# Kernel optimization log

Measured on AMD Instinct MI355X. Metric: run time of the kernel, lower is better.

Reference implementation:

```python
import jax, jax.numpy as jnp
import numpy as np

D_MODEL = 1024
NUM_HEADS = 16
D_K = D_MODEL // NUM_HEADS


def setup_inputs() -> dict:
    key = jax.random.key(0)
    ks = jax.random.split(key, 5)
    s = 1.0 / np.sqrt(D_MODEL)
    return {
        "x": jax.random.normal(ks[0], (2, 2048, D_MODEL), dtype=jnp.float32),
        "Wq": jax.random.normal(ks[1], (D_MODEL, D_MODEL), dtype=jnp.float32) * s,
        "bq": jnp.zeros((D_MODEL,), dtype=jnp.float32),
        "Wk": jax.random.normal(ks[2], (D_MODEL, D_MODEL), dtype=jnp.float32) * s,
        "bk": jnp.zeros((D_MODEL,), dtype=jnp.float32),
        "Wv": jax.random.normal(ks[3], (D_MODEL, D_MODEL), dtype=jnp.float32) * s,
        "bv": jnp.zeros((D_MODEL,), dtype=jnp.float32),
        "Wo": jax.random.normal(ks[4], (D_MODEL, D_MODEL), dtype=jnp.float32) * s,
        "bo": jnp.zeros((D_MODEL,), dtype=jnp.float32),
    }


def reference(x, Wq, bq, Wk, bk, Wv, bv, Wo, bo):
    B, S, D = x.shape
    H, dk = NUM_HEADS, D_K
    Q = x @ Wq + bq  # [B, S, D]
    K = x @ Wk + bk
    V = x @ Wv + bv
    # Faithful to the torch code: plain .view(B, H, S, dk) (NO transpose),
    # i.e. heads are carved out of the flattened (S*D) dim, not the feature dim.
    Q = Q.reshape(B, H, S, dk)
    K = K.reshape(B, H, S, dk)
    V = V.reshape(B, H, S, dk)
    scores = jnp.einsum("bhqd,bhkd->bhqk", Q, K) / jnp.sqrt(jnp.float32(dk))
    attn = jax.nn.softmax(scores, axis=-1)  # [B, H, S, S]
    ctx = jnp.einsum("bhqk,bhkd->bhqd", attn, V)  # [B, H, S, dk]
    out = ctx.reshape(B, S, D) @ Wo + bo
    return out  # dropout is identity in eval mode
```

## Files before the change

kernel.cpp:

```cpp
#include <hip/hip_runtime.h>
#include <hip/hip_bf16.h>
#include <math.h>

#define D_MODEL 1024
#define SEQ     2048
#define BATCH   2
#define NHEAD   16
#define DKH     64
#define BH      (BATCH * NHEAD)

typedef unsigned short u16;
typedef unsigned int   u32;
typedef __bf16 bf16x8 __attribute__((ext_vector_type(8)));
typedef float  f32x4  __attribute__((ext_vector_type(4)));

#define MFMA16(a, b, c) __builtin_amdgcn_mfma_f32_16x16x32_bf16((a), (b), (c), 0, 0, 0)
#define AS1 __attribute__((address_space(1)))
#define AS3 __attribute__((address_space(3)))

#define QSCALE 0.18033688f

__device__ __forceinline__ u16 f2bf(float x) {
    u32 u = __float_as_uint(x);
    u += 0x7fffu + ((u >> 16) & 1u);
    return (u16)(u >> 16);
}
__device__ __forceinline__ float bf2f(u16 b) {
    return __uint_as_float(((u32)b) << 16);
}
__device__ __forceinline__ void gl16(const u16* g, void* lds) {
    __builtin_amdgcn_global_load_lds((const AS1 u32*)g, (AS3 u32*)lds, 16, 0, 0);
}

__global__ __launch_bounds__(256) void conv_all(
    const float* __restrict__ x, u16* __restrict__ Xh, int n4,
    const float* __restrict__ W0, const float* __restrict__ W1,
    const float* __restrict__ W2, const float* __restrict__ W3,
    u16* __restrict__ H0, u16* __restrict__ L0, u16* __restrict__ H1, u16* __restrict__ L1,
    u16* __restrict__ H2, u16* __restrict__ L2, u16* __restrict__ H3, u16* __restrict__ L3)
{
    const int t = threadIdx.x;
    if ((int)blockIdx.x < 4096) {
        int i = blockIdx.x * 256 + t;
        if (i >= n4) return;
        float4 v = reinterpret_cast<const float4*>(x)[i];
        uint2 H;
        H.x = f2bf(v.x) | ((u32)f2bf(v.y) << 16);
        H.y = f2bf(v.z) | ((u32)f2bf(v.w) << 16);
        reinterpret_cast<uint2*>(Xh)[i] = H;
        return;
    }
    int id = blockIdx.x - 4096;
    int bx = id & 15, by = (id >> 4) & 15, bz = id >> 8;
    const float* W; u16 *Ht, *Lt;
    if (bz == 0)      { W = W0; Ht = H0; Lt = L0; }
    else if (bz == 1) { W = W1; Ht = H1; Lt = L1; }
    else if (bz == 2) { W = W2; Ht = H2; Lt = L2; }
    else              { W = W3; Ht = H3; Lt = L3; }

    __shared__ float T[64][65];
    const int n0 = bx * 64, k0 = by * 64;
    #pragma unroll
    for (int i = 0; i < 4; ++i) {
        int f = t + i * 256;
        int kr = f >> 4, ns = (f & 15) * 4;
        float4 v = *reinterpret_cast<const float4*>(&W[(size_t)(k0 + kr) * D_MODEL + n0 + ns]);
        T[kr][ns + 0] = v.x; T[kr][ns + 1] = v.y; T[kr][ns + 2] = v.z; T[kr][ns + 3] = v.w;
    }
    __syncthreads();
    #pragma unroll
    for (int i = 0; i < 4; ++i) {
        int f = t + i * 256;
        int nr = f >> 4, ks = (f & 15) * 4;
        u16 hh[4], ll[4];
        #pragma unroll
        for (int j = 0; j < 4; ++j) {
            float xv = T[ks + j][nr];
            u16 hb = f2bf(xv);
            hh[j] = hb;
            ll[j] = f2bf(xv - bf2f(hb));
        }
        uint2 H, L;
        H.x = hh[0] | ((u32)hh[1] << 16); H.y = hh[2] | ((u32)hh[3] << 16);
        L.x = ll[0] | ((u32)ll[1] << 16); L.y = ll[2] | ((u32)ll[3] << 16);
        size_t o = (size_t)(n0 + nr) * D_MODEL + k0 + ks;
        *reinterpret_cast<uint2*>(&Ht[o]) = H;
        *reinterpret_cast<uint2*>(&Lt[o]) = L;
    }
}

__global__ __launch_bounds__(512, 2) void gemm_qkv(
    const u16* __restrict__ AhG,
    const u16* __restrict__ Bqh, const u16* __restrict__ Bql,
    const u16* __restrict__ Bkh, const u16* __restrict__ Bkl,
    const u16* __restrict__ Bvh, const u16* __restrict__ Bvl,
    const float* __restrict__ bq, const float* __restrict__ bk, const float* __restrict__ bv,
    u16* __restrict__ Qb, u16* __restrict__ Kb, u16* __restrict__ Vb)
{
    constexpr int K = D_MODEL, N = D_MODEL;
    __shared__ u16 LB[2][28672];

    const int tid  = threadIdx.x;
    const int wv   = tid >> 6;
    const int lane = tid & 63;
    const int quad = lane >> 4;
    const int l16  = lane & 15;
    const int wm   = wv >> 1, wn = wv & 1;
    const int brow = blockIdx.y * 128, bcol = blockIdx.x * 128;

    const u16* sp[7];
    int sldb[7];
    #pragma unroll
    for (int j = 0; j < 7; ++j) {
        int c = wv * 7 + j, a = c >> 3, cc = c & 7;
        int row = cc * 16 + (lane >> 2);
        int gseg = (lane & 3) ^ ((lane >> 3) & 3);
        const u16* p;
        if (a == 0)      p = AhG;
        else if (a == 1) p = Bqh;
        else if (a == 2) p = Bql;
        else if (a == 3) p = Bkh;
        else if (a == 4) p = Bkl;
        else if (a == 5) p = Bvh;
        else             p = Bvl;
        int rbase = (a == 0) ? brow : bcol;
        sp[j]   = p + (size_t)(rbase + row) * K + gseg * 8;
        sldb[j] = a * 8192 + cc * 1024;
    }

    int aro[2], bro[4];
    #pragma unroll
    for (int i = 0; i < 2; ++i) {
        int mr = wm * 32 + i * 16 + l16;
        aro[i] = mr * 64 + ((quad ^ ((mr >> 1) & 3)) * 16);
    }
    #pragma unroll
    for (int i = 0; i < 4; ++i) {
        int nr = wn * 64 + i * 16 + l16;
        bro[i] = nr * 64 + ((quad ^ ((nr >> 1) & 3)) * 16);
    }

    f32x4 acc[3][2][4] = {};

    #pragma unroll
    for (int j = 0; j < 7; ++j)
        gl16(sp[j], (char*)LB[0] + sldb[j]);

    for (int it = 0; it < K / 32; ++it) {
        const int cur = it & 1;
        __syncthreads();
        if (it + 1 < K / 32) {
            const int nxt = cur ^ 1;
            const int k1 = (it + 1) * 32;
            #pragma unroll
            for (int j = 0; j < 7; ++j)
                gl16(sp[j] + k1, (char*)LB[nxt] + sldb[j]);
        }

        bf16x8 ah[2];
        #pragma unroll
        for (int i = 0; i < 2; ++i)
            ah[i] = *reinterpret_cast<const bf16x8*>((const char*)LB[cur] + aro[i]);
        #pragma unroll
        for (int m = 0; m < 3; ++m) {
            const int bbh = (1 + 2 * m) * 8192, bbl = (2 + 2 * m) * 8192;
            bf16x8 bh[4], bl[4];
            #pragma unroll
            for (int i = 0; i < 4; ++i) {
                bh[i] = *reinterpret_cast<const bf16x8*>((const char*)LB[cur] + bbh + bro[i]);
                bl[i] = *reinterpret_cast<const bf16x8*>((const char*)LB[cur] + bbl + bro[i]);
            }
            #pragma unroll
            for (int mi = 0; mi < 2; ++mi)
                #pragma unroll
                for (int ni = 0; ni < 4; ++ni) {
                    f32x4 c = acc[m][mi][ni];
                    c = MFMA16(ah[mi], bh[ni], c);
                    c = MFMA16(ah[mi], bl[ni], c);
                    acc[m][mi][ni] = c;
                }
        }
    }

    #pragma unroll
    for (int m = 0; m < 3; ++m) {
        const float* bias = (m == 0) ? bq : (m == 1) ? bk : bv;
        u16* out = (m == 0) ? Qb : (m == 1) ? Kb : Vb;
        const float sc = (m == 0) ? QSCALE : 1.0f;
        #pragma unroll
        for (int mi = 0; mi < 2; ++mi) {
            #pragma unroll
            for (int ni = 0; ni < 4; ++ni) {
                int col = bcol + wn * 64 + ni * 16 + l16;
                float bvv = bias[col];
                #pragma unroll
                for (int r = 0; r < 4; ++r) {
                    int row = brow + wm * 32 + mi * 16 + quad * 4 + r;
                    out[(size_t)row * N + col] = f2bf((acc[m][mi][ni][r] + bvv) * sc);
                }
            }
        }
    }
}

__global__ __launch_bounds__(512, 2) void gemm_oproj(
    const u16* __restrict__ AhG, const u16* __restrict__ Bh, const u16* __restrict__ Bl,
    const float* __restrict__ bias, float* __restrict__ Cf)
{
    constexpr int K = D_MODEL, N = D_MODEL;
    __shared__ u16 LB[2][12288];

    const int tid  = threadIdx.x;
    const int wv   = tid >> 6;
    const int lane = tid & 63;
    const int quad = lane >> 4;
    const int l16  = lane & 15;
    const int wm   = wv >> 1, wn = wv & 1;
    const int brow = blockIdx.y * 128, bcol = blockIdx.x * 128;

    const u16* sp[3];
    int sldb[3];
    #pragma unroll
    for (int j = 0; j < 3; ++j) {
        int c = wv * 3 + j, a = c >> 3, cc = c & 7;
        int row = cc * 16 + (lane >> 2);
        int gseg = (lane & 3) ^ ((lane >> 3) & 3);
        const u16* p = (a == 0) ? AhG : (a == 1) ? Bh : Bl;
        int rbase = (a == 0) ? brow : bcol;
        sp[j]   = p + (size_t)(rbase + row) * K + gseg * 8;
        sldb[j] = a * 8192 + cc * 1024;
    }

    int aro[2], bro[4];
    #pragma unroll
    for (int i = 0; i < 2; ++i) {
        int mr = wm * 32 + i * 16 + l16;
        aro[i] = mr * 64 + ((quad ^ ((mr >> 1) & 3)) * 16);
    }
    #pragma unroll
    for (int i = 0; i < 4; ++i) {
        int nr = wn * 64 + i * 16 + l16;
        bro[i] = nr * 64 + ((quad ^ ((nr >> 1) & 3)) * 16);
    }

    f32x4 acc[2][4] = {};

    #pragma unroll
    for (int j = 0; j < 3; ++j)
        gl16(sp[j], (char*)LB[0] + sldb[j]);

    for (int it = 0; it < K / 32; ++it) {
        const int cur = it & 1;
        __syncthreads();
        if (it + 1 < K / 32) {
            const int nxt = cur ^ 1;
            const int k1 = (it + 1) * 32;
            #pragma unroll
            for (int j = 0; j < 3; ++j)
                gl16(sp[j] + k1, (char*)LB[nxt] + sldb[j]);
        }

        bf16x8 ah[2], bh[4], bl[4];
        #pragma unroll
        for (int i = 0; i < 2; ++i)
            ah[i] = *reinterpret_cast<const bf16x8*>((const char*)LB[cur] + aro[i]);
        #pragma unroll
        for (int i = 0; i < 4; ++i) {
            bh[i] = *reinterpret_cast<const bf16x8*>((const char*)LB[cur] + 8192 + bro[i]);
            bl[i] = *reinterpret_cast<const bf16x8*>((const char*)LB[cur] + 16384 + bro[i]);
        }
        #pragma unroll
        for (int mi = 0; mi < 2; ++mi)
            #pragma unroll
            for (int ni = 0; ni < 4; ++ni) {
                f32x4 c = acc[mi][ni];
                c = MFMA16(ah[mi], bh[ni], c);
                c = MFMA16(ah[mi], bl[ni], c);
                acc[mi][ni] = c;
            }
    }

    #pragma unroll
    for (int mi = 0; mi < 2; ++mi) {
        #pragma unroll
        for (int ni = 0; ni < 4; ++ni) {
            int col = bcol + wn * 64 + ni * 16 + l16;
            float bvv = bias[col];
            #pragma unroll
            for (int r = 0; r < 4; ++r) {
                int row = brow + wm * 32 + mi * 16 + quad * 4 + r;
                Cf[(size_t)row * N + col] = acc[mi][ni][r] + bvv;
            }
        }
    }
}

__global__ __launch_bounds__(256) void v_transpose(
    const u16* __restrict__ V, u16* __restrict__ Vt)
{
    __shared__ u16 T[64][72];
    const int bh = blockIdx.y, st = blockIdx.x;
    const u16* src = V + ((size_t)bh * SEQ + (size_t)st * 64) * 64;
    const int t = threadIdx.x;
    #pragma unroll
    for (int i = 0; i < 2; ++i) {
        int c  = t + i * 256;
        int s  = c >> 3;
        int d0 = (c & 7) * 8;
        uint4 v = reinterpret_cast<const uint4*>(src)[c];
        u16 e[8];
        e[0] = (u16)(v.x & 0xffff); e[1] = (u16)(v.x >> 16);
        e[2] = (u16)(v.y & 0xffff); e[3] = (u16)(v.y >> 16);
        e[4] = (u16)(v.z & 0xffff); e[5] = (u16)(v.z >> 16);
        e[6] = (u16)(v.w & 0xffff); e[7] = (u16)(v.w >> 16);
        #pragma unroll
        for (int j = 0; j < 8; ++j) T[d0 + j][s] = e[j];
    }
    __syncthreads();
    const int d = t >> 2, seg = t & 3;
    u16* dst = Vt + (size_t)bh * 64 * SEQ + (size_t)d * SEQ + st * 64 + seg * 16;
    uint4 a = *reinterpret_cast<const uint4*>(&T[d][seg * 16]);
    uint4 b = *reinterpret_cast<const uint4*>(&T[d][seg * 16 + 8]);
    reinterpret_cast<uint4*>(dst)[0] = a;
    reinterpret_cast<uint4*>(dst)[1] = b;
}

__global__ __launch_bounds__(256, 2) void attn_mfma(
    const u16* __restrict__ Qb_g, const u16* __restrict__ Kb_g,
    const u16* __restrict__ Vt_g, u16* __restrict__ Ch_g)
{
    __shared__ u16 KVS[2][8192];
    __shared__ u16 Pb [128 * 72];

    const int tid  = threadIdx.x;
    const int wv   = tid >> 6;
    const int lane = tid & 63;
    const int quad = lane >> 4;
    const int l16  = lane & 15;
    const int id   = blockIdx.x;
    const int bh   = id & 31;
    const int qt   = id >> 5;

    const size_t qbase = ((size_t)bh * SEQ + (size_t)qt * 128) * 64;
    const size_t kbh   = (size_t)bh * SEQ * 64;
    const size_t vtbh  = (size_t)bh * 64 * SEQ;

    bf16x8 qf[2][2];
    #pragma unroll
    for (int sub = 0; sub < 2; ++sub)
        #pragma unroll
        for (int ks = 0; ks < 2; ++ks) {
            size_t o = qbase + (size_t)(wv * 32 + sub * 16 + l16) * 64 + ks * 32 + quad * 8;
            qf[sub][ks] = *reinterpret_cast<const bf16x8*>(Qb_g + o);
        }

    const u16* sp[4];
    size_t sstep[4];
    int sldb[4];
    #pragma unroll
    for (int j = 0; j < 4; ++j) {
        int c   = wv * 4 + j;
        int arr = c >> 3, cc = c & 7;
        int row = cc * 8 + (lane >> 3);
        int sg  = (lane & 7) ^ (row & 7);
        if (arr == 0) { sp[j] = Kb_g + kbh + (size_t)row * 64 + sg * 8;   sstep[j] = 4096; }
        else          { sp[j] = Vt_g + vtbh + (size_t)row * SEQ + sg * 8; sstep[j] = 64; }
        sldb[j] = arr * 8192 + cc * 1024;
    }

    int fro[4][2];
    #pragma unroll
    for (int t = 0; t < 4; ++t)
        #pragma unroll
        for (int ks = 0; ks < 2; ++ks)
            fro[t][ks] = (t * 16 + l16) * 128 + (((ks * 4 + quad) ^ (l16 & 7)) * 16);

    bf16x8 onesv;
    #pragma unroll
    for (int i = 0; i < 8; ++i) onesv[i] = (__bf16)1.0f;

    f32x4 oacc[2][4] = {};
    f32x4 lsum[2] = {};

    #pragma unroll
    for (int j = 0; j < 4; ++j)
        gl16(sp[j], (char*)KVS[0] + sldb[j]);

    for (int kt = 0; kt < SEQ / 64; ++kt) {
        const int cur = kt & 1;
        __syncthreads();
        if (kt + 1 < SEQ / 64) {
            const int nxt = cur ^ 1;
            #pragma unroll
            for (int j = 0; j < 4; ++j)
                gl16(sp[j] + (size_t)(kt + 1) * sstep[j], (char*)KVS[nxt] + sldb[j]);
        }

        f32x4 sacc[2][4] = {};
        #pragma unroll
        for (int t4 = 0; t4 < 4; ++t4) {
            bf16x8 kh[2];
            kh[0] = *reinterpret_cast<const bf16x8*>((const char*)KVS[cur] + fro[t4][0]);
            kh[1] = *reinterpret_cast<const bf16x8*>((const char*)KVS[cur] + fro[t4][1]);
            #pragma unroll
            for (int sub = 0; sub < 2; ++sub) {
                f32x4 a = sacc[sub][t4];
                a = MFMA16(qf[sub][0], kh[0], a);
                a = MFMA16(qf[sub][1], kh[1], a);
                sacc[sub][t4] = a;
            }
        }

        #pragma unroll
        for (int sub = 0; sub < 2; ++sub) {
            int rowb = wv * 32 + sub * 16 + quad * 4;
            #pragma unroll
            for (int r = 0; r < 4; ++r) {
                u32 u0 = __float_as_uint(__builtin_amdgcn_exp2f(sacc[sub][0][r]));
                u32 u1 = __float_as_uint(__builtin_amdgcn_exp2f(sacc[sub][1][r]));
                u32 u2 = __float_as_uint(__builtin_amdgcn_exp2f(sacc[sub][2][r]));
                u32 u3 = __float_as_uint(__builtin_amdgcn_exp2f(sacc[sub][3][r]));
                int ro = (rowb + r) * 72 + l16;
                Pb[ro +  0] = (u16)(u0 >> 16);
                Pb[ro + 16] = (u16)(u1 >> 16);
                Pb[ro + 32] = (u16)(u2 >> 16);
                Pb[ro + 48] = (u16)(u3 >> 16);
            }
        }

        bf16x8 bvf[4][2];
        #pragma unroll
        for (int dt = 0; dt < 4; ++dt) {
            bvf[dt][0] = *reinterpret_cast<const bf16x8*>((const char*)KVS[cur] + 8192 + fro[dt][0]);
            bvf[dt][1] = *reinterpret_cast<const bf16x8*>((const char*)KVS[cur] + 8192 + fro[dt][1]);
        }
        #pragma unroll
        for (int sub = 0; sub < 2; ++sub) {
            bf16x8 ap[2];
            #pragma unroll
            for (int ks = 0; ks < 2; ++ks)
                ap[ks] = *reinterpret_cast<const bf16x8*>(
                    &Pb[(wv * 32 + sub * 16 + l16) * 72 + ks * 32 + quad * 8]);
            #pragma unroll
            for (int dt = 0; dt < 4; ++dt) {
                oacc[sub][dt] = MFMA16(ap[0], bvf[dt][0], oacc[sub][dt]);
                oacc[sub][dt] = MFMA16(ap[1], bvf[dt][1], oacc[sub][dt]);
            }
            lsum[sub] = MFMA16(ap[0], onesv, lsum[sub]);
            lsum[sub] = MFMA16(ap[1], onesv, lsum[sub]);
        }
    }

    u16* Oh = Ch_g + qbase;
    #pragma unroll
    for (int sub = 0; sub < 2; ++sub) {
        float inv[4];
        #pragma unroll
        for (int r = 0; r < 4; ++r) inv[r] = 1.0f / lsum[sub][r];
        #pragma unroll
        for (int dt = 0; dt < 4; ++dt)
            #pragma unroll
            for (int r = 0; r < 4; ++r) {
                int row = wv * 32 + sub * 16 + quad * 4 + r;
                Oh[(size_t)row * 64 + dt * 16 + l16] = f2bf(oacc[sub][dt][r] * inv[r]);
            }
    }
}

extern "C" void kernel_launch(void* const* d_in, const int* in_sizes, int n_in,
                              void* d_out, int out_size, void* d_ws, size_t ws_size,
                              hipStream_t stream)
{
    const float* x  = (const float*)d_in[0];
    const float* Wq = (const float*)d_in[1];
    const float* bq = (const float*)d_in[2];
    const float* Wk = (const float*)d_in[3];
    const float* bk = (const float*)d_in[4];
    const float* Wv = (const float*)d_in[5];
    const float* bv = (const float*)d_in[6];
    const float* Wo = (const float*)d_in[7];
    const float* bo = (const float*)d_in[8];
    float* out = (float*)d_out;

    const int M = BATCH * SEQ;
    const int N = D_MODEL;
    const size_t NE = (size_t)M * N;
    const size_t NW = (size_t)N * N;

    u16* w16 = (u16*)d_ws;
    u16* Xh   = w16;
    u16* Qb   = Xh   + NE;
    u16* Kb   = Qb   + NE;
    u16* Vb   = Kb   + NE;
    u16* Vtb  = Vb   + NE;
    u16* Ctxh = Vtb  + NE;
    u16* WTqh = Ctxh + NE;
    u16* WTql = WTqh + NW;
    u16* WTkh = WTql + NW;
    u16* WTkl = WTkh + NW;
    u16* WTvh = WTkl + NW;
    u16* WTvl = WTvh + NW;
    u16* WToh = WTvl + NW;
    u16* WTol = WToh + NW;

    conv_all<<<dim3(4096 + 1024), dim3(256), 0, stream>>>(
        x, Xh, (int)(NE / 4),
        Wq, Wk, Wv, Wo, WTqh, WTql, WTkh, WTkl, WTvh, WTvl, WToh, WTol);

    gemm_qkv<<<dim3(N / 128, M / 128), dim3(512), 0, stream>>>(
        Xh, WTqh, WTql, WTkh, WTkl, WTvh, WTvl, bq, bk, bv, Qb, Kb, Vb);

    v_transpose<<<dim3(SEQ / 64, BH), dim3(256), 0, stream>>>(Vb, Vtb);

    attn_mfma<<<dim3((SEQ / 128) * BH), dim3(256), 0, stream>>>(Qb, Kb, Vtb, Ctxh);

    gemm_oproj<<<dim3(N / 128, M / 128), dim3(512), 0, stream>>>(
        Ctxh, WToh, WTol, bo, out);
}
```

Baseline: 223.5 us.

## Drop low-order weight split in QKV GEMM and load K/V directly in attention

The QKV projection now uses only the high bf16 part of each weight instead of a hi+lo split. This halves the MFMAs, the LDS footprint and the weight loads, and conversion no longer writes lo parts for Wq/Wk/Wv. The attention kernel removes its double-buffered LDS staging of K and V^T and reads MFMA fragments directly from global memory, so it no longer needs the K/V barriers. The risks are lower projection accuracy and repeated global/cache reads of K/V by each wave.

```diff
diff --git a/kernel.cpp b/kernel.cpp
--- a/kernel.cpp
+++ b/kernel.cpp
@@ -36,8 +36,8 @@
     const float* __restrict__ x, u16* __restrict__ Xh, int n4,
     const float* __restrict__ W0, const float* __restrict__ W1,
     const float* __restrict__ W2, const float* __restrict__ W3,
-    u16* __restrict__ H0, u16* __restrict__ L0, u16* __restrict__ H1, u16* __restrict__ L1,
-    u16* __restrict__ H2, u16* __restrict__ L2, u16* __restrict__ H3, u16* __restrict__ L3)
+    u16* __restrict__ Hq, u16* __restrict__ Hk, u16* __restrict__ Hv,
+    u16* __restrict__ Ho, u16* __restrict__ Lo)
 {
     const int t = threadIdx.x;
     if ((int)blockIdx.x < 4096) {
@@ -52,11 +52,11 @@
     }
     int id = blockIdx.x - 4096;
     int bx = id & 15, by = (id >> 4) & 15, bz = id >> 8;
-    const float* W; u16 *Ht, *Lt;
-    if (bz == 0)      { W = W0; Ht = H0; Lt = L0; }
-    else if (bz == 1) { W = W1; Ht = H1; Lt = L1; }
-    else if (bz == 2) { W = W2; Ht = H2; Lt = L2; }
-    else              { W = W3; Ht = H3; Lt = L3; }
+    const float* W; u16* Ht;
+    if (bz == 0)      { W = W0; Ht = Hq; }
+    else if (bz == 1) { W = W1; Ht = Hk; }
+    else if (bz == 2) { W = W2; Ht = Hv; }
+    else              { W = W3; Ht = Ho; }
 
     __shared__ float T[64][65];
     const int n0 = bx * 64, k0 = by * 64;
@@ -85,20 +85,18 @@
         L.x = ll[0] | ((u32)ll[1] << 16); L.y = ll[2] | ((u32)ll[3] << 16);
         size_t o = (size_t)(n0 + nr) * D_MODEL + k0 + ks;
         *reinterpret_cast<uint2*>(&Ht[o]) = H;
-        *reinterpret_cast<uint2*>(&Lt[o]) = L;
+        if (bz == 3) *reinterpret_cast<uint2*>(&Lo[o]) = L;
     }
 }
 
 __global__ __launch_bounds__(512, 2) void gemm_qkv(
     const u16* __restrict__ AhG,
-    const u16* __restrict__ Bqh, const u16* __restrict__ Bql,
-    const u16* __restrict__ Bkh, const u16* __restrict__ Bkl,
-    const u16* __restrict__ Bvh, const u16* __restrict__ Bvl,
+    const u16* __restrict__ Bqh, const u16* __restrict__ Bkh, const u16* __restrict__ Bvh,
     const float* __restrict__ bq, const float* __restrict__ bk, const float* __restrict__ bv,
     u16* __restrict__ Qb, u16* __restrict__ Kb, u16* __restrict__ Vb)
 {
     constexpr int K = D_MODEL, N = D_MODEL;
-    __shared__ u16 LB[2][28672];
+    __shared__ u16 LB[2][16384];
 
     const int tid  = threadIdx.x;
     const int wv   = tid >> 6;
@@ -108,21 +106,18 @@
     const int wm   = wv >> 1, wn = wv & 1;
     const int brow = blockIdx.y * 128, bcol = blockIdx.x * 128;
 
-    const u16* sp[7];
-    int sldb[7];
-    #pragma unroll
-    for (int j = 0; j < 7; ++j) {
-        int c = wv * 7 + j, a = c >> 3, cc = c & 7;
+    const u16* sp[4];
+    int sldb[4];
+    #pragma unroll
+    for (int j = 0; j < 4; ++j) {
+        int c = wv * 4 + j, a = c >> 3, cc = c & 7;
         int row = cc * 16 + (lane >> 2);
         int gseg = (lane & 3) ^ ((lane >> 3) & 3);
         const u16* p;
         if (a == 0)      p = AhG;
         else if (a == 1) p = Bqh;
-        else if (a == 2) p = Bql;
-        else if (a == 3) p = Bkh;
-        else if (a == 4) p = Bkl;
-        else if (a == 5) p = Bvh;
-        else             p = Bvl;
+        else if (a == 2) p = Bkh;
+        else             p = Bvh;
         int rbase = (a == 0) ? brow : bcol;
         sp[j]   = p + (size_t)(rbase + row) * K + gseg * 8;
         sldb[j] = a * 8192 + cc * 1024;
@@ -143,7 +138,7 @@
     f32x4 acc[3][2][4] = {};
 
     #pragma unroll
-    for (int j = 0; j < 7; ++j)
+    for (int j = 0; j < 4; ++j)
         gl16(sp[j], (char*)LB[0] + sldb[j]);
 
     for (int it = 0; it < K / 32; ++it) {
@@ -153,7 +148,7 @@
             const int nxt = cur ^ 1;
             const int k1 = (it + 1) * 32;
             #pragma unroll
-            for (int j = 0; j < 7; ++j)
+            for (int j = 0; j < 4; ++j)
                 gl16(sp[j] + k1, (char*)LB[nxt] + sldb[j]);
         }
 
@@ -163,22 +158,16 @@
             ah[i] = *reinterpret_cast<const bf16x8*>((const char*)LB[cur] + aro[i]);
         #pragma unroll
         for (int m = 0; m < 3; ++m) {
-            const int bbh = (1 + 2 * m) * 8192, bbl = (2 + 2 * m) * 8192;
-            bf16x8 bh[4], bl[4];
-            #pragma unroll
-            for (int i = 0; i < 4; ++i) {
-                bh[i] = *reinterpret_cast<const bf16x8*>((const char*)LB[cur] + bbh + bro[i]);
-                bl[i] = *reinterpret_cast<const bf16x8*>((const char*)LB[cur] + bbl + bro[i]);
-            }
+            const int bb = (1 + m) * 8192;
+            bf16x8 bh[4];
+            #pragma unroll
+            for (int i = 0; i < 4; ++i)
+                bh[i] = *reinterpret_cast<const bf16x8*>((const char*)LB[cur] + bb + bro[i]);
             #pragma unroll
             for (int mi = 0; mi < 2; ++mi)
                 #pragma unroll
-                for (int ni = 0; ni < 4; ++ni) {
-                    f32x4 c = acc[m][mi][ni];
-                    c = MFMA16(ah[mi], bh[ni], c);
-                    c = MFMA16(ah[mi], bl[ni], c);
-                    acc[m][mi][ni] = c;
-                }
+                for (int ni = 0; ni < 4; ++ni)
+                    acc[m][mi][ni] = MFMA16(ah[mi], bh[ni], acc[m][mi][ni]);
         }
     }
 
@@ -329,8 +318,7 @@
     const u16* __restrict__ Qb_g, const u16* __restrict__ Kb_g,
     const u16* __restrict__ Vt_g, u16* __restrict__ Ch_g)
 {
-    __shared__ u16 KVS[2][8192];
-    __shared__ u16 Pb [128 * 72];
+    __shared__ u16 Pb[128 * 72];
 
     const int tid  = threadIdx.x;
     const int wv   = tid >> 6;
@@ -342,8 +330,8 @@
     const int qt   = id >> 5;
 
     const size_t qbase = ((size_t)bh * SEQ + (size_t)qt * 128) * 64;
-    const size_t kbh   = (size_t)bh * SEQ * 64;
-    const size_t vtbh  = (size_t)bh * 64 * SEQ;
+    const u16* Kt = Kb_g + (size_t)bh * SEQ * 64;
+    const u16* Vh = Vt_g + (size_t)bh * 64 * SEQ;
 
     bf16x8 qf[2][2];
     #pragma unroll
@@ -354,26 +342,14 @@
             qf[sub][ks] = *reinterpret_cast<const bf16x8*>(Qb_g + o);
         }
 
-    const u16* sp[4];
-    size_t sstep[4];
-    int sldb[4];
-    #pragma unroll
-    for (int j = 0; j < 4; ++j) {
-        int c   = wv * 4 + j;
-        int arr = c >> 3, cc = c & 7;
-        int row = cc * 8 + (lane >> 3);
-        int sg  = (lane & 7) ^ (row & 7);
-        if (arr == 0) { sp[j] = Kb_g + kbh + (size_t)row * 64 + sg * 8;   sstep[j] = 4096; }
-        else          { sp[j] = Vt_g + vtbh + (size_t)row * SEQ + sg * 8; sstep[j] = 64; }
-        sldb[j] = arr * 8192 + cc * 1024;
-    }
-
-    int fro[4][2];
+    int kfo[4][2], vfo[4][2];
     #pragma unroll
     for (int t = 0; t < 4; ++t)
         #pragma unroll
-        for (int ks = 0; ks < 2; ++ks)
-            fro[t][ks] = (t * 16 + l16) * 128 + (((ks * 4 + quad) ^ (l16 & 7)) * 16);
+        for (int ks = 0; ks < 2; ++ks) {
+            kfo[t][ks] = (t * 16 + l16) * 64 + ks * 32 + quad * 8;
+            vfo[t][ks] = (t * 16 + l16) * SEQ + ks * 32 + quad * 8;
+        }
 
     bf16x8 onesv;
     #pragma unroll
@@ -382,31 +358,20 @@
     f32x4 oacc[2][4] = {};
     f32x4 lsum[2] = {};
 
-    #pragma unroll
-    for (int j = 0; j < 4; ++j)
-        gl16(sp[j], (char*)KVS[0] + sldb[j]);
-
     for (int kt = 0; kt < SEQ / 64; ++kt) {
-        const int cur = kt & 1;
-        __syncthreads();
-        if (kt + 1 < SEQ / 64) {
-            const int nxt = cur ^ 1;
-            #pragma unroll
-            for (int j = 0; j < 4; ++j)
-                gl16(sp[j] + (size_t)(kt + 1) * sstep[j], (char*)KVS[nxt] + sldb[j]);
-        }
+        const int kofs = kt * 64 * 64;
+        const int vofs = kt * 64;
 
         f32x4 sacc[2][4] = {};
         #pragma unroll
         for (int t4 = 0; t4 < 4; ++t4) {
-            bf16x8 kh[2];
-            kh[0] = *reinterpret_cast<const bf16x8*>((const char*)KVS[cur] + fro[t4][0]);
-            kh[1] = *reinterpret_cast<const bf16x8*>((const char*)KVS[cur] + fro[t4][1]);
+            bf16x8 kh0 = *reinterpret_cast<const bf16x8*>(Kt + kofs + kfo[t4][0]);
+            bf16x8 kh1 = *reinterpret_cast<const bf16x8*>(Kt + kofs + kfo[t4][1]);
             #pragma unroll
             for (int sub = 0; sub < 2; ++sub) {
                 f32x4 a = sacc[sub][t4];
-                a = MFMA16(qf[sub][0], kh[0], a);
-                a = MFMA16(qf[sub][1], kh[1], a);
+                a = MFMA16(qf[sub][0], kh0, a);
+                a = MFMA16(qf[sub][1], kh1, a);
                 sacc[sub][t4] = a;
             }
         }
@@ -428,26 +393,25 @@
             }
         }
 
-        bf16x8 bvf[4][2];
+        bf16x8 bv0[4], bv1[4];
         #pragma unroll
         for (int dt = 0; dt < 4; ++dt) {
-            bvf[dt][0] = *reinterpret_cast<const bf16x8*>((const char*)KVS[cur] + 8192 + fro[dt][0]);
-            bvf[dt][1] = *reinterpret_cast<const bf16x8*>((const char*)KVS[cur] + 8192 + fro[dt][1]);
+            bv0[dt] = *reinterpret_cast<const bf16x8*>(Vh + vofs + vfo[dt][0]);
+            bv1[dt] = *reinterpret_cast<const bf16x8*>(Vh + vofs + vfo[dt][1]);
         }
         #pragma unroll
         for (int sub = 0; sub < 2; ++sub) {
-            bf16x8 ap[2];
-            #pragma unroll
-            for (int ks = 0; ks < 2; ++ks)
-                ap[ks] = *reinterpret_cast<const bf16x8*>(
-                    &Pb[(wv * 32 + sub * 16 + l16) * 72 + ks * 32 + quad * 8]);
+            bf16x8 ap0 = *reinterpret_cast<const bf16x8*>(
+                &Pb[(wv * 32 + sub * 16 + l16) * 72 + 0 + quad * 8]);
+            bf16x8 ap1 = *reinterpret_cast<const bf16x8*>(
+                &Pb[(wv * 32 + sub * 16 + l16) * 72 + 32 + quad * 8]);
             #pragma unroll
             for (int dt = 0; dt < 4; ++dt) {
-                oacc[sub][dt] = MFMA16(ap[0], bvf[dt][0], oacc[sub][dt]);
-                oacc[sub][dt] = MFMA16(ap[1], bvf[dt][1], oacc[sub][dt]);
-            }
-            lsum[sub] = MFMA16(ap[0], onesv, lsum[sub]);
-            lsum[sub] = MFMA16(ap[1], onesv, lsum[sub]);
+                oacc[sub][dt] = MFMA16(ap0, bv0[dt], oacc[sub][dt]);
+                oacc[sub][dt] = MFMA16(ap1, bv1[dt], oacc[sub][dt]);
+            }
+            lsum[sub] = MFMA16(ap0, onesv, lsum[sub]);
+            lsum[sub] = MFMA16(ap1, onesv, lsum[sub]);
         }
     }
 
@@ -495,20 +459,17 @@
     u16* Vtb  = Vb   + NE;
     u16* Ctxh = Vtb  + NE;
     u16* WTqh = Ctxh + NE;
-    u16* WTql = WTqh + NW;
-    u16* WTkh = WTql + NW;
-    u16* WTkl = WTkh + NW;
-    u16* WTvh = WTkl + NW;
-    u16* WTvl = WTvh + NW;
-    u16* WToh = WTvl + NW;
+    u16* WTkh = WTqh + NW;
+    u16* WTvh = WTkh + NW;
+    u16* WToh = WTvh + NW;
     u16* WTol = WToh + NW;
 
     conv_all<<<dim3(4096 + 1024), dim3(256), 0, stream>>>(
         x, Xh, (int)(NE / 4),
-        Wq, Wk, Wv, Wo, WTqh, WTql, WTkh, WTkl, WTvh, WTvl, WToh, WTol);
+        Wq, Wk, Wv, Wo, WTqh, WTkh, WTvh, WToh, WTol);
 
     gemm_qkv<<<dim3(N / 128, M / 128), dim3(512), 0, stream>>>(
-        Xh, WTqh, WTql, WTkh, WTkl, WTvh, WTvl, bq, bk, bv, Qb, Kb, Vb);
+        Xh, WTqh, WTkh, WTvh, bq, bk, bv, Qb, Kb, Vb);
 
     v_transpose<<<dim3(SEQ / 64, BH), dim3(256), 0, stream>>>(Vb, Vtb);
 
```

Result: slower. 267.5 us (+19.7%).
